# Kernel optimization log

Measured on AMD Instinct MI355X. Metric: run time of the kernel, lower is better.

Reference implementation:

```python
import jax, jax.numpy as jnp
import numpy as np

MASK_VALUE = -1000000.0


def setup_inputs() -> dict:
    key = jax.random.key(0)
    k1, k2, k3, k4 = jax.random.split(key, 4)
    B, Lq, Lk, d = 32, 1024, 1024, 128
    return {
        "query": jax.random.normal(k1, (B, Lq, d), dtype=jnp.float32),
        "key": jax.random.normal(k2, (B, Lk, d), dtype=jnp.float32),
        "value": jax.random.normal(k3, (B, Lk, d), dtype=jnp.float32),
        "valid_length": jax.random.randint(k4, (B,), 0, Lk, dtype=jnp.int64),
    }


def reference(query, key, value, valid_length):
    # query [B, Lq, d], key/value [B, Lk, d], valid_length [B]
    d = query.shape[-1]
    # scores [B, Lq, Lk]
    scores = jnp.einsum("bqd,bkd->bqk", query, key) / jnp.sqrt(jnp.float32(d))
    Lk = key.shape[1]
    # mask positions >= valid_length with -1e6 (per-batch, broadcast over Lq)
    pos = jnp.arange(Lk)  # [Lk]
    mask = pos[None, None, :] >= valid_length[:, None, None]  # [B, 1, Lk]
    scores = jnp.where(mask, MASK_VALUE, scores)
    attn = jax.nn.softmax(scores, axis=-1)
    # dropout p=0.0 in eval -> identity
    return jnp.einsum("bqk,bkd->bqd", attn, value)
```

## Files before the change

kernel.cpp:

```cpp
#include <hip/hip_runtime.h>

#define B_N 32
#define LQ  1024
#define LK  1024
#define DH  128

typedef __attribute__((ext_vector_type(4))) float    f32x4;
typedef __attribute__((ext_vector_type(8))) short    s16x8;
typedef __attribute__((ext_vector_type(4))) _Float16 f16x4;
typedef __attribute__((ext_vector_type(8))) _Float16 f16x8;

__device__ inline unsigned short f2bf(float f) {
    union { float f; unsigned u; } c; c.f = f;
    unsigned u = c.u;
    u += 0x7fffu + ((u >> 16) & 1u);
    return (unsigned short)(u >> 16);
}

#define ESCALE 0.12751743f

__global__ __launch_bounds__(256)
void prep_kv(const float* __restrict__ K, const float* __restrict__ V,
             unsigned short* __restrict__ Kb, _Float16* __restrict__ Vt)
{
    __shared__ float tl[32 * 132];
    const int tid  = threadIdx.x;
    const int lane = tid & 63;
    const int wv   = tid >> 6;
    const int n    = lane & 15;
    const int quad = lane >> 4;

    const bool isK = blockIdx.x < 1024;
    const int  t   = isK ? blockIdx.x : (blockIdx.x - 1024);
    const int  b   = t >> 5, kt = t & 31;

    const float4* src = (const float4*)((isK ? K : V) + ((size_t)b * LK + kt * 32) * DH);
    #pragma unroll
    for (int h = 0; h < 4; ++h) {
        const int idx = h * 256 + tid;
        const int row = idx >> 5, c4 = idx & 31;
        *(float4*)&tl[row * 132 + c4 * 4] = src[idx];
    }
    __syncthreads();

    if (isK) {
        union { s16x8 v; unsigned short u[8]; } t8;
        #pragma unroll
        for (int h = 0; h < 2; ++h) {
            const int f = wv * 2 + h;
            const int tt2 = f >> 2, s = f & 3;
            const float* p = &tl[(tt2 * 16 + n) * 132 + s * 32 + quad * 8];
            const float4 a = *(const float4*)p;
            const float4 c = *(const float4*)(p + 4);
            t8.u[0] = f2bf(a.x); t8.u[1] = f2bf(a.y); t8.u[2] = f2bf(a.z); t8.u[3] = f2bf(a.w);
            t8.u[4] = f2bf(c.x); t8.u[5] = f2bf(c.y); t8.u[6] = f2bf(c.z); t8.u[7] = f2bf(c.w);
            const int w = b * 256 + (kt * 2 + tt2) * 4 + s;
            *(s16x8*)(Kb + (size_t)w * 512 + lane * 8) = t8.v;
        }
    } else {
        #pragma unroll
        for (int h = 0; h < 2; ++h) {
            const int f  = wv * 2 + h;
            const int kg = f >> 2, dp = f & 3;
            f16x8 t8;
            #pragma unroll
            for (int i = 0; i < 4; ++i) {
                const float* row = &tl[(kg * 16 + quad * 4 + i) * 132 + dp * 32 + n];
                t8[i]     = (_Float16)row[0];
                t8[4 + i] = (_Float16)row[16];
            }
            const int v = (b * 64 + kt * 2 + kg) * 4 + dp;
            *(f16x8*)(Vt + (size_t)v * 512 + lane * 8) = t8;
        }
    }
}

__global__ __launch_bounds__(64)
void attn_fwd(const float* __restrict__ Q, const unsigned short* __restrict__ Kb,
              const _Float16* __restrict__ Vt, const int* __restrict__ VL,
              float* __restrict__ O)
{
    const int lane = threadIdx.x & 63;
    const int quad = lane >> 4;
    const int m16  = lane & 15;

    const int b  = blockIdx.x & 31;
    const int qt = blockIdx.x >> 5;
    const int q0 = qt * 16;

    const int vl = VL[b];
    const int nch = (vl > 0) ? ((vl + 63) >> 6) : 16;
    const float emaskval = (vl == 0) ? 1.0f : 0.0f;

    s16x8 qf[4];
    {
        const float* qrow = Q + ((size_t)b * LQ + q0 + m16) * DH + quad * 8;
        #pragma unroll
        for (int s = 0; s < 4; ++s) {
            const float4 a = *(const float4*)(qrow + s * 32);
            const float4 c = *(const float4*)(qrow + s * 32 + 4);
            union { s16x8 v; unsigned short u[8]; } t;
            t.u[0] = f2bf(a.x); t.u[1] = f2bf(a.y); t.u[2] = f2bf(a.z); t.u[3] = f2bf(a.w);
            t.u[4] = f2bf(c.x); t.u[5] = f2bf(c.y); t.u[6] = f2bf(c.z); t.u[7] = f2bf(c.w);
            qf[s] = t.v;
        }
    }

    f32x4 o[8];
    #pragma unroll
    for (int dt = 0; dt < 8; ++dt) o[dt] = (f32x4){0.f, 0.f, 0.f, 0.f};
    float lrun = 0.f;

    const unsigned short* kbase = Kb + (size_t)b * (256 * 512) + lane * 8;
    const _Float16*       vbase = Vt + (size_t)b * (256 * 512) + lane * 8;

    s16x8 kf[16];
    f16x8 vp[16];
    #pragma unroll
    for (int i = 0; i < 16; ++i) kf[i] = *(const s16x8*)(kbase + i * 512);
    #pragma unroll
    for (int i = 0; i < 16; ++i) vp[i] = *(const f16x8*)(vbase + i * 512);

    for (int kb = 0; kb < nch; ++kb) {
        f32x4 st[4];
        #pragma unroll
        for (int g = 0; g < 4; ++g) st[g] = (f32x4){0.f, 0.f, 0.f, 0.f};
        #pragma unroll
        for (int g = 0; g < 4; ++g) {
            #pragma unroll
            for (int s = 0; s < 4; ++s)
                st[g] = __builtin_amdgcn_mfma_f32_16x16x32_bf16(kf[g * 4 + s], qf[s], st[g], 0, 0, 0);
        }

        const int knx = (kb + 1 < nch) ? (kb + 1) : kb;
        const unsigned short* kcn = kbase + (size_t)knx * (16 * 512);
        #pragma unroll
        for (int i = 0; i < 16; ++i) kf[i] = *(const s16x8*)(kcn + i * 512);

        const bool maskc = (kb * 64 + 64 > vl);
        f16x4 pA[4];
        #pragma unroll
        for (int g = 0; g < 4; ++g) {
            float e[4];
            #pragma unroll
            for (int i = 0; i < 4; ++i) {
                e[i] = __builtin_amdgcn_exp2f(st[g][i] * ESCALE);
                if (maskc && (kb * 64 + g * 16 + quad * 4 + i >= vl)) e[i] = emaskval;
            }
            lrun += (e[0] + e[1]) + (e[2] + e[3]);
            pA[g] = (f16x4){(_Float16)e[0], (_Float16)e[1], (_Float16)e[2], (_Float16)e[3]};
        }

        #pragma unroll
        for (int g = 0; g < 4; ++g) {
            #pragma unroll
            for (int dp = 0; dp < 4; ++dp) {
                const f16x8 w  = vp[g * 4 + dp];
                const f16x4 lo = __builtin_shufflevector(w, w, 0, 1, 2, 3);
                const f16x4 hi = __builtin_shufflevector(w, w, 4, 5, 6, 7);
                o[dp * 2]     = __builtin_amdgcn_mfma_f32_16x16x16f16(pA[g], lo, o[dp * 2],     0, 0, 0);
                o[dp * 2 + 1] = __builtin_amdgcn_mfma_f32_16x16x16f16(pA[g], hi, o[dp * 2 + 1], 0, 0, 0);
            }
        }

        const _Float16* vcn = vbase + (size_t)knx * (16 * 512);
        #pragma unroll
        for (int i = 0; i < 16; ++i) vp[i] = *(const f16x8*)(vcn + i * 512);
    }

    float L = lrun;
    L += __shfl_xor(L, 16);
    L += __shfl_xor(L, 32);
    const size_t obase = ((size_t)b * LQ + q0 + quad * 4) * DH + m16;
    #pragma unroll
    for (int r = 0; r < 4; ++r) {
        const float inv = 1.0f / __shfl(L, quad * 4 + r);
        #pragma unroll
        for (int dt = 0; dt < 8; ++dt)
            O[obase + (size_t)r * DH + dt * 16] = o[dt][r] * inv;
    }
}

extern "C" void kernel_launch(void* const* d_in, const int* in_sizes, int n_in,
                              void* d_out, int out_size, void* d_ws, size_t ws_size,
                              hipStream_t stream) {
    const float* Q  = (const float*)d_in[0];
    const float* K  = (const float*)d_in[1];
    const float* V  = (const float*)d_in[2];
    const int*   VL = (const int*)d_in[3];
    float* O = (float*)d_out;
    (void)in_sizes; (void)n_in; (void)out_size; (void)ws_size;

    unsigned short* Kb = (unsigned short*)d_ws;
    _Float16*       Vt = (_Float16*)(Kb + (size_t)B_N * 256 * 512);

    prep_kv<<<dim3(2048), dim3(256), 0, stream>>>(K, V, Kb, Vt);
    attn_fwd<<<dim3(B_N * (LQ / 16)), dim3(64), 0, stream>>>(Q, Kb, Vt, VL, O);
}
```

Measured before the change: 131.2 us.

## Split key chunks across two waves with 32-query tiles and LDS reduction

Each block now processes 32 queries in two 16-row halves, and its two waves take alternating 64-key chunks (split-K). Every K/V fragment loaded now feeds two query tiles, which halves K/V traffic per query. The two waves' partial outputs and row sums are combined through shared memory before normalising. This is valid without a running max because the kernel already uses unnormalised exp. In exchange, register pressure roughly doubles (two accumulator sets and two query fragment sets), there are half as many blocks, and an extra LDS exchange and barrier are added at the end.

```diff
diff --git a/kernel.cpp b/kernel.cpp
--- a/kernel.cpp
+++ b/kernel.cpp
@@ -75,26 +75,32 @@
     }
 }
 
-__global__ __launch_bounds__(64)
+__global__ __launch_bounds__(128, 2)
 void attn_fwd(const float* __restrict__ Q, const unsigned short* __restrict__ Kb,
               const _Float16* __restrict__ Vt, const int* __restrict__ VL,
               float* __restrict__ O)
 {
-    const int lane = threadIdx.x & 63;
+    __shared__ f32x4 Om[2][8][64];
+    __shared__ float Lm[2][64];
+
+    const int tid  = threadIdx.x;
+    const int lane = tid & 63;
+    const int wv   = tid >> 6;
     const int quad = lane >> 4;
     const int m16  = lane & 15;
 
     const int b  = blockIdx.x & 31;
-    const int qt = blockIdx.x >> 5;
-    const int q0 = qt * 16;
+    const int qg = blockIdx.x >> 5;
+    const int q0 = qg * 32;
 
     const int vl = VL[b];
     const int nch = (vl > 0) ? ((vl + 63) >> 6) : 16;
     const float emaskval = (vl == 0) ? 1.0f : 0.0f;
 
-    s16x8 qf[4];
-    {
-        const float* qrow = Q + ((size_t)b * LQ + q0 + m16) * DH + quad * 8;
+    s16x8 qf[2][4];
+    #pragma unroll
+    for (int h = 0; h < 2; ++h) {
+        const float* qrow = Q + ((size_t)b * LQ + q0 + h * 16 + m16) * DH + quad * 8;
         #pragma unroll
         for (int s = 0; s < 4; ++s) {
             const float4 a = *(const float4*)(qrow + s * 32);
@@ -102,54 +108,59 @@
             union { s16x8 v; unsigned short u[8]; } t;
             t.u[0] = f2bf(a.x); t.u[1] = f2bf(a.y); t.u[2] = f2bf(a.z); t.u[3] = f2bf(a.w);
             t.u[4] = f2bf(c.x); t.u[5] = f2bf(c.y); t.u[6] = f2bf(c.z); t.u[7] = f2bf(c.w);
-            qf[s] = t.v;
-        }
-    }
-
-    f32x4 o[8];
-    #pragma unroll
-    for (int dt = 0; dt < 8; ++dt) o[dt] = (f32x4){0.f, 0.f, 0.f, 0.f};
-    float lrun = 0.f;
+            qf[h][s] = t.v;
+        }
+    }
+
+    f32x4 o[2][8];
+    #pragma unroll
+    for (int h = 0; h < 2; ++h)
+        #pragma unroll
+        for (int dt = 0; dt < 8; ++dt) o[h][dt] = (f32x4){0.f, 0.f, 0.f, 0.f};
+    float lrun[2] = {0.f, 0.f};
 
     const unsigned short* kbase = Kb + (size_t)b * (256 * 512) + lane * 8;
     const _Float16*       vbase = Vt + (size_t)b * (256 * 512) + lane * 8;
 
     s16x8 kf[16];
     f16x8 vp[16];
-    #pragma unroll
-    for (int i = 0; i < 16; ++i) kf[i] = *(const s16x8*)(kbase + i * 512);
-    #pragma unroll
-    for (int i = 0; i < 16; ++i) vp[i] = *(const f16x8*)(vbase + i * 512);
-
-    for (int kb = 0; kb < nch; ++kb) {
-        f32x4 st[4];
-        #pragma unroll
-        for (int g = 0; g < 4; ++g) st[g] = (f32x4){0.f, 0.f, 0.f, 0.f};
+    if (wv < nch) {
+        const unsigned short* kc = kbase + (size_t)wv * (16 * 512);
+        const _Float16*       vc = vbase + (size_t)wv * (16 * 512);
+        #pragma unroll
+        for (int i = 0; i < 16; ++i) kf[i] = *(const s16x8*)(kc + i * 512);
+        #pragma unroll
+        for (int i = 0; i < 16; ++i) vp[i] = *(const f16x8*)(vc + i * 512);
+    }
+
+    for (int kb = wv; kb < nch; kb += 2) {
+        int knx = kb + 2; if (knx >= nch) knx = kb;
+
+        const bool maskc = (kb * 64 + 64 > vl);
+        f16x4 pA[2][4];
         #pragma unroll
         for (int g = 0; g < 4; ++g) {
-            #pragma unroll
-            for (int s = 0; s < 4; ++s)
-                st[g] = __builtin_amdgcn_mfma_f32_16x16x32_bf16(kf[g * 4 + s], qf[s], st[g], 0, 0, 0);
-        }
-
-        const int knx = (kb + 1 < nch) ? (kb + 1) : kb;
+            f32x4 st0 = (f32x4){0.f, 0.f, 0.f, 0.f};
+            f32x4 st1 = (f32x4){0.f, 0.f, 0.f, 0.f};
+            #pragma unroll
+            for (int s = 0; s < 4; ++s) {
+                st0 = __builtin_amdgcn_mfma_f32_16x16x32_bf16(kf[g * 4 + s], qf[0][s], st0, 0, 0, 0);
+                st1 = __builtin_amdgcn_mfma_f32_16x16x32_bf16(kf[g * 4 + s], qf[1][s], st1, 0, 0, 0);
+            }
+            #pragma unroll
+            for (int i = 0; i < 4; ++i) {
+                float e0 = __builtin_amdgcn_exp2f(st0[i] * ESCALE);
+                float e1 = __builtin_amdgcn_exp2f(st1[i] * ESCALE);
+                if (maskc && (kb * 64 + g * 16 + quad * 4 + i >= vl)) { e0 = emaskval; e1 = emaskval; }
+                lrun[0] += e0; lrun[1] += e1;
+                pA[0][g][i] = (_Float16)e0;
+                pA[1][g][i] = (_Float16)e1;
+            }
+        }
+
         const unsigned short* kcn = kbase + (size_t)knx * (16 * 512);
         #pragma unroll
         for (int i = 0; i < 16; ++i) kf[i] = *(const s16x8*)(kcn + i * 512);
-
-        const bool maskc = (kb * 64 + 64 > vl);
-        f16x4 pA[4];
-        #pragma unroll
-        for (int g = 0; g < 4; ++g) {
-            float e[4];
-            #pragma unroll
-            for (int i = 0; i < 4; ++i) {
-                e[i] = __builtin_amdgcn_exp2f(st[g][i] * ESCALE);
-                if (maskc && (kb * 64 + g * 16 + quad * 4 + i >= vl)) e[i] = emaskval;
-            }
-            lrun += (e[0] + e[1]) + (e[2] + e[3]);
-            pA[g] = (f16x4){(_Float16)e[0], (_Float16)e[1], (_Float16)e[2], (_Float16)e[3]};
-        }
 
         #pragma unroll
         for (int g = 0; g < 4; ++g) {
@@ -158,8 +169,10 @@
                 const f16x8 w  = vp[g * 4 + dp];
                 const f16x4 lo = __builtin_shufflevector(w, w, 0, 1, 2, 3);
                 const f16x4 hi = __builtin_shufflevector(w, w, 4, 5, 6, 7);
-                o[dp * 2]     = __builtin_amdgcn_mfma_f32_16x16x16f16(pA[g], lo, o[dp * 2],     0, 0, 0);
-                o[dp * 2 + 1] = __builtin_amdgcn_mfma_f32_16x16x16f16(pA[g], hi, o[dp * 2 + 1], 0, 0, 0);
+                o[0][dp * 2]     = __builtin_amdgcn_mfma_f32_16x16x16f16(pA[0][g], lo, o[0][dp * 2],     0, 0, 0);
+                o[0][dp * 2 + 1] = __builtin_amdgcn_mfma_f32_16x16x16f16(pA[0][g], hi, o[0][dp * 2 + 1], 0, 0, 0);
+                o[1][dp * 2]     = __builtin_amdgcn_mfma_f32_16x16x16f16(pA[1][g], lo, o[1][dp * 2],     0, 0, 0);
+                o[1][dp * 2 + 1] = __builtin_amdgcn_mfma_f32_16x16x16f16(pA[1][g], hi, o[1][dp * 2 + 1], 0, 0, 0);
             }
         }
 
@@ -168,16 +181,25 @@
         for (int i = 0; i < 16; ++i) vp[i] = *(const f16x8*)(vcn + i * 512);
     }
 
-    float L = lrun;
+    const int oh = 1 - wv;
+    #pragma unroll
+    for (int dt = 0; dt < 8; ++dt) Om[wv][dt][lane] = o[oh][dt];
+    Lm[wv][lane] = lrun[oh];
+    __syncthreads();
+    f32x4 om[8];
+    #pragma unroll
+    for (int dt = 0; dt < 8; ++dt) om[dt] = o[wv][dt] + Om[oh][dt][lane];
+    float L = lrun[wv] + Lm[oh][lane];
+
     L += __shfl_xor(L, 16);
     L += __shfl_xor(L, 32);
-    const size_t obase = ((size_t)b * LQ + q0 + quad * 4) * DH + m16;
+    const size_t obase = ((size_t)b * LQ + q0 + wv * 16 + quad * 4) * DH + m16;
     #pragma unroll
     for (int r = 0; r < 4; ++r) {
         const float inv = 1.0f / __shfl(L, quad * 4 + r);
         #pragma unroll
         for (int dt = 0; dt < 8; ++dt)
-            O[obase + (size_t)r * DH + dt * 16] = o[dt][r] * inv;
+            O[obase + (size_t)r * DH + dt * 16] = om[dt][r] * inv;
     }
 }
 
@@ -195,5 +217,5 @@
     _Float16*       Vt = (_Float16*)(Kb + (size_t)B_N * 256 * 512);
 
     prep_kv<<<dim3(2048), dim3(256), 0, stream>>>(K, V, Kb, Vt);
-    attn_fwd<<<dim3(B_N * (LQ / 16)), dim3(64), 0, stream>>>(Q, Kb, Vt, VL, O);
-}
+    attn_fwd<<<dim3(B_N * (LQ / 32)), dim3(128), 0, stream>>>(Q, Kb, Vt, VL, O);
+}
```

Result: slower. 148.1 us (+12.9%).
